# Kernel optimization log

Measured on AMD Instinct MI355X. Metric: run time of the kernel, lower is better.

## Reference

```python
import jax, jax.numpy as jnp
import numpy as np

KERNEL = 7
PAD = (KERNEL - 1) // 2


def setup_inputs() -> dict:
    key = jax.random.key(0)
    k1, k2 = jax.random.split(key)
    x = jax.random.normal(k1, (32, 256, 64, 64), dtype=jnp.float32)
    W = jax.random.normal(k2, (1, 2, KERNEL, KERNEL), dtype=jnp.float32) * 0.1
    return {"x": x, "W": W}


def reference(x, W):
    # channel-wise max and mean pooling -> [B, 2, H, W]
    x_compress = jnp.concatenate(
        [jnp.max(x, axis=1, keepdims=True), jnp.mean(x, axis=1, keepdims=True)],
        axis=1,
    )
    # 2->1 conv, same padding, no bias/bn/relu
    attn = jax.lax.conv_general_dilated(
        x_compress, W,
        window_strides=(1, 1),
        padding=[(PAD, PAD), (PAD, PAD)],
        dimension_numbers=("NCHW", "OIHW", "NCHW"),
    )
    scale = jax.nn.sigmoid(attn)  # [B, 1, H, W]
    return x * scale
```

## Files before the change

### kernel.cpp

```cpp
#include <hip/hip_runtime.h>
#include <math.h>

#define BB 32
#define CC 256
#define HH 64
#define WW 64
#define HWSZ 4096
#define CHW 1048576

__global__ void sg_reduce(const float* __restrict__ x,
                          float* __restrict__ maxp,
                          float* __restrict__ meanp) {
    int t = blockIdx.x * blockDim.x + threadIdx.x;
    int b  = t >> 11;
    int s2 = t & 2047;
    const float2* xp = reinterpret_cast<const float2*>(x + (size_t)b * CHW) + s2;
    float2 v = xp[0];
    float2 mx = v;
    float2 sm = v;
    #pragma unroll 8
    for (int c = 1; c < CC; ++c) {
        float2 u = xp[(size_t)c * (HWSZ / 2)];
        mx.x = fmaxf(mx.x, u.x); mx.y = fmaxf(mx.y, u.y);
        sm.x += u.x;             sm.y += u.y;
    }
    reinterpret_cast<float2*>(maxp)[t] = mx;
    float2 mn;
    mn.x = sm.x * (1.0f / CC);
    mn.y = sm.y * (1.0f / CC);
    reinterpret_cast<float2*>(meanp)[t] = mn;
}

__global__ void sg_conv(const float* __restrict__ maxp,
                        const float* __restrict__ meanp,
                        const float* __restrict__ Wt,
                        float* __restrict__ scale) {
    __shared__ float w[98];
    int lt = threadIdx.x;
    if (lt < 98) w[lt] = Wt[lt];
    __syncthreads();

    int t = blockIdx.x * blockDim.x + lt;
    int b = t >> 12;
    int s = t & 4095;
    int h = s >> 6;
    int wc = s & 63;
    const float* mb = maxp  + b * HWSZ;
    const float* nb = meanp + b * HWSZ;

    float acc = 0.0f;
    #pragma unroll
    for (int kh = 0; kh < 7; ++kh) {
        int hh = h + kh - 3;
        if ((unsigned)hh >= (unsigned)HH) continue;
        #pragma unroll
        for (int kw = 0; kw < 7; ++kw) {
            int wcol = wc + kw - 3;
            if ((unsigned)wcol >= (unsigned)WW) continue;
            int o = (hh << 6) + wcol;
            acc = fmaf(mb[o], w[kh * 7 + kw],      acc);
            acc = fmaf(nb[o], w[49 + kh * 7 + kw], acc);
        }
    }
    scale[t] = 1.0f / (1.0f + __expf(-acc));
}

__global__ void sg_apply(const float* __restrict__ x,
                         const float* __restrict__ scale,
                         float* __restrict__ out) {
    const int total4 = BB * CHW / 4;
    int stride = gridDim.x * blockDim.x;
    for (int i = blockIdx.x * blockDim.x + threadIdx.x; i < total4; i += stride) {
        float4 v = reinterpret_cast<const float4*>(x)[i];
        int b  = i >> 18;
        int s4 = i & 1023;
        float4 sc = reinterpret_cast<const float4*>(scale)[(b << 10) + s4];
        v.x *= sc.x; v.y *= sc.y; v.z *= sc.z; v.w *= sc.w;
        reinterpret_cast<float4*>(out)[i] = v;
    }
}

extern "C" void kernel_launch(void* const* d_in, const int* in_sizes, int n_in,
                              void* d_out, int out_size, void* d_ws, size_t ws_size,
                              hipStream_t stream) {
    const float* x  = (const float*)d_in[0];
    const float* Wt = (const float*)d_in[1];
    float* out = (float*)d_out;

    float* wsf   = (float*)d_ws;
    float* maxp  = wsf;
    float* meanp = wsf + BB * HWSZ;
    float* scale = wsf + 2 * BB * HWSZ;

    sg_reduce<<<(BB * HWSZ / 2) / 256, 256, 0, stream>>>(x, maxp, meanp);
    sg_conv<<<(BB * HWSZ) / 256, 256, 0, stream>>>(maxp, meanp, Wt, scale);
    sg_apply<<<2048, 256, 0, stream>>>(x, scale, out);
}
```

Measured before the change: 87.85 us.

## Split channel reduction across threads with shared-memory combine

The channel max/mean reduction now gives each block one (batch,row) pair, and 16 channel groups of 16 threads each reduce 16 channels with float4 loads. Partial results are combined through shared memory. Before, each thread walked all 256 channels serially with float2 loads. The new version raises memory-level parallelism from 256 blocks to 2048, at the cost of a sync, an LDS combine, and 16-wide row segments per load.

```diff
diff --git a/kernel.cpp b/kernel.cpp
--- a/kernel.cpp
+++ b/kernel.cpp
@@ -11,24 +11,48 @@
 __global__ void sg_reduce(const float* __restrict__ x,
                           float* __restrict__ maxp,
                           float* __restrict__ meanp) {
-    int t = blockIdx.x * blockDim.x + threadIdx.x;
-    int b  = t >> 11;
-    int s2 = t & 2047;
-    const float2* xp = reinterpret_cast<const float2*>(x + (size_t)b * CHW) + s2;
-    float2 v = xp[0];
-    float2 mx = v;
-    float2 sm = v;
-    #pragma unroll 8
-    for (int c = 1; c < CC; ++c) {
-        float2 u = xp[(size_t)c * (HWSZ / 2)];
+    int bh = blockIdx.x;
+    int b  = bh >> 6;
+    int h  = bh & 63;
+    int w4 = threadIdx.x & 15;
+    int cg = threadIdx.x >> 4;
+
+    const float4* base =
+        reinterpret_cast<const float4*>(x + (size_t)b * CHW + h * WW) + w4;
+    float4 v = base[(size_t)(cg * 16) * 1024];
+    float4 mx = v, sm = v;
+    #pragma unroll
+    for (int cc = 1; cc < 16; ++cc) {
+        float4 u = base[(size_t)(cg * 16 + cc) * 1024];
         mx.x = fmaxf(mx.x, u.x); mx.y = fmaxf(mx.y, u.y);
-        sm.x += u.x;             sm.y += u.y;
+        mx.z = fmaxf(mx.z, u.z); mx.w = fmaxf(mx.w, u.w);
+        sm.x += u.x; sm.y += u.y; sm.z += u.z; sm.w += u.w;
     }
-    reinterpret_cast<float2*>(maxp)[t] = mx;
-    float2 mn;
-    mn.x = sm.x * (1.0f / CC);
-    mn.y = sm.y * (1.0f / CC);
-    reinterpret_cast<float2*>(meanp)[t] = mn;
+
+    __shared__ float4 lmax[16][16];
+    __shared__ float4 lsum[16][16];
+    lmax[cg][w4] = mx;
+    lsum[cg][w4] = sm;
+    __syncthreads();
+
+    if (threadIdx.x < 16) {
+        int w = threadIdx.x;
+        float4 M = lmax[0][w];
+        float4 S = lsum[0][w];
+        #pragma unroll
+        for (int g = 1; g < 16; ++g) {
+            float4 m2 = lmax[g][w];
+            float4 s2 = lsum[g][w];
+            M.x = fmaxf(M.x, m2.x); M.y = fmaxf(M.y, m2.y);
+            M.z = fmaxf(M.z, m2.z); M.w = fmaxf(M.w, m2.w);
+            S.x += s2.x; S.y += s2.y; S.z += s2.z; S.w += s2.w;
+        }
+        reinterpret_cast<float4*>(maxp)[bh * 16 + w] = M;
+        float4 mn;
+        mn.x = S.x * (1.0f / CC); mn.y = S.y * (1.0f / CC);
+        mn.z = S.z * (1.0f / CC); mn.w = S.w * (1.0f / CC);
+        reinterpret_cast<float4*>(meanp)[bh * 16 + w] = mn;
+    }
 }
 
 __global__ void sg_conv(const float* __restrict__ maxp,
@@ -92,7 +116,7 @@
     float* meanp = wsf + BB * HWSZ;
     float* scale = wsf + 2 * BB * HWSZ;
 
-    sg_reduce<<<(BB * HWSZ / 2) / 256, 256, 0, stream>>>(x, maxp, meanp);
+    sg_reduce<<<BB * HH, 256, 0, stream>>>(x, maxp, meanp);
     sg_conv<<<(BB * HWSZ) / 256, 256, 0, stream>>>(maxp, meanp, Wt, scale);
     sg_apply<<<2048, 256, 0, stream>>>(x, scale, out);
 }
```

Result: faster. 75.19 us (-14.4%).
